# Performance work log

Measured on AMD Instinct MI355X. Metric: run time of the kernel, lower is better.

## Reference

```python
import jax, jax.numpy as jnp
import numpy as np
from jax import lax

B, C_IN, C_OUT, K, H, W, NUM = 32, 256, 256, 3, 28, 28, 8


def setup_inputs() -> dict:
    key = jax.random.key(0)
    k1, k2, k3 = jax.random.split(key, 3)
    inputs = jax.random.normal(k1, (B, C_IN, H, W), dtype=jnp.float32)
    inputs_se = jax.random.uniform(k2, (B, NUM), dtype=jnp.float32)
    # weight bank [out*in*k*k, num], init scale sqrt(1/(c*k*k)) as in the module
    scale = np.sqrt(1.0 / (C_IN * K * K)).astype(np.float32)
    weight = jax.random.normal(k3, (C_OUT * C_IN * K * K, NUM), dtype=jnp.float32) * scale
    bias = jnp.zeros((C_OUT,), dtype=jnp.float32)
    return {"inputs": inputs, "inputs_se": inputs_se, "weight": weight, "bias": bias}


def reference(inputs, inputs_se, weight, bias):
    b, c, h, w = inputs.shape
    out_ch = bias.shape[0]
    # per-sample filter generation: [B, num] @ [num, out*in*k*k] -> [B, out, in, k, k]
    wgen = jnp.einsum('bn,on->bo', inputs_se, weight).reshape(b, out_ch, c, K, K)

    def conv_one(x, wk):
        # x: [C,H,W], wk: [O,C,K,K] -> [O,H,W]  (stride 1, padding 1)
        return lax.conv_general_dilated(
            x[None], wk,
            window_strides=(1, 1), padding=[(1, 1), (1, 1)],
            dimension_numbers=('NCHW', 'OIHW', 'NCHW'))[0]

    out = jax.vmap(conv_one)(inputs, wgen)  # [B, O, H, W]
    return out + bias[None, :, None, None]
```

## Files before the change

kernel.cpp:

```cpp
#include <hip/hip_runtime.h>
#include <hip/hip_fp16.h>

#define BB    32
#define CIN   256
#define COUT  256
#define HH    28
#define WW    28
#define NPIX  784
#define HP    30
#define WP    30

#define BM    128
#define BN    128
#define NT    7

#define SLICE_ELEMS 294912
#define WGEN_ELEMS  ((size_t)BB * 2 * SLICE_ELEMS)
#define XPAD_OFF    (WGEN_ELEMS)

#define PREP_GENW  256
#define PREP_GENX  960
#define PREP_GRID  (PREP_GENW + PREP_GENX)

typedef _Float16 f16x8 __attribute__((ext_vector_type(8)));
typedef float    f32x4 __attribute__((ext_vector_type(4)));

static __device__ __forceinline__ ushort f2h_bits(float v) {
    __half h = __float2half(v);
    return *reinterpret_cast<ushort*>(&h);
}

static __device__ __forceinline__ void gll16(const ushort* g, ushort* l) {
    __builtin_amdgcn_global_load_lds(
        (const __attribute__((address_space(1))) unsigned int*)g,
        (__attribute__((address_space(3))) unsigned int*)l, 16, 0, 0);
}

__global__ __launch_bounds__(256) void prep(const float* __restrict__ weight,
                                            const float* __restrict__ se,
                                            const float* __restrict__ x,
                                            ushort* __restrict__ wgen2,
                                            ushort* __restrict__ xpad) {
    __shared__ __align__(16) char smem[29696];
    const int bid = blockIdx.x;
    const int tid = threadIdx.x;

    if (bid < PREP_GENW) {
        const int og  = bid >> 3;
        const int c32 = bid & 7;
        const int ol  = tid >> 5;
        const int cl  = tid & 31;
        const int o   = og * 8 + ol;
        const int c   = c32 * 32 + cl;
        const int mt  = o >> 7;
        const int sub = (o >> 4) & 7;
        const int col = o & 15;

        float*  se_sh = (float*)smem;
        ushort* w_lds = (ushort*)(smem + 1024);

        se_sh[tid] = se[tid];

        float4 wr[18];
        const float4* wp = (const float4*)(weight + ((size_t)o * CIN + c) * 72);
#pragma unroll
        for (int i = 0; i < 18; ++i) wr[i] = wp[i];

        const int khw0 = tid >> 5;
        const int q0   = (tid >> 3) & 3;
        const int ol0  = tid & 7;
        const int khw1 = 8;
        const int q1   = (tid >> 3) & 3;
        const int ol1  = tid & 7;
        const int o0   = og * 8 + ol0;
        const int sub0 = (o0 >> 4) & 7, col0 = o0 & 15;
        const int o1   = og * 8 + ol1;
        const int sub1 = (o1 >> 4) & 7, col1 = o1 & 15;
        const int dst0 = ((c32 * 9 + khw0) * 512 + sub0 * 64 + q0 * 16 + col0) * 8;
        const int dst1 = ((c32 * 9 + khw1) * 512 + sub1 * 64 + q1 * 16 + col1) * 8;
        const int src0 = (khw0 * 8 + ol0) * 40 + q0 * 8;
        const int src1 = (khw1 * 8 + ol1) * 40 + q1 * 8;

        __syncthreads();

        for (int b = 0; b < BB; ++b) {
            const float s0 = se_sh[b * 8 + 0], s1 = se_sh[b * 8 + 1];
            const float s2 = se_sh[b * 8 + 2], s3 = se_sh[b * 8 + 3];
            const float s4 = se_sh[b * 8 + 4], s5 = se_sh[b * 8 + 5];
            const float s6 = se_sh[b * 8 + 6], s7 = se_sh[b * 8 + 7];
#pragma unroll
            for (int k = 0; k < 9; ++k) {
                const float4 w0 = wr[2 * k + 0];
                const float4 w1 = wr[2 * k + 1];
                const float v = w0.x * s0 + w0.y * s1 + w0.z * s2 + w0.w * s3
                              + w1.x * s4 + w1.y * s5 + w1.z * s6 + w1.w * s7;
                w_lds[(k * 8 + ol) * 40 + cl] = f2h_bits(v);
            }
            __syncthreads();
            ushort* slice_base = wgen2 + (size_t)(b * 2 + mt) * SLICE_ELEMS;
            *(uint4*)(slice_base + dst0) = *(const uint4*)(w_lds + src0);
            if (tid < 32)
                *(uint4*)(slice_base + dst1) = *(const uint4*)(w_lds + src1);
            __syncthreads();
        }
    } else {
        const int idx = bid - PREP_GENW;
        const int hp  = idx % HP;
        const int b   = idx / HP;
        ushort* row = xpad + ((size_t)b * HP + hp) * WP * CIN;

        if (hp == 0 || hp == HP - 1) {
            uint* r32 = (uint*)row;
            for (int i = tid; i < (WP * CIN) / 2; i += 256) r32[i] = 0u;
            return;
        }
        {
            uint* c0 = (uint*)row;
            uint* c1 = (uint*)(row + (WP - 1) * CIN);
            if (tid < 128)       c0[tid] = 0u;
            else                 c1[tid - 128] = 0u;
        }
        float* lds = (float*)smem;
        const int h = hp - 1;
        const float* xr = x + (size_t)b * CIN * NPIX + h * WW;

        for (int f = tid; f < CIN * WW; f += 256) {
            const int c = f / WW;
            const int w = f % WW;
            lds[c * (WW + 1) + w] = xr[(size_t)c * NPIX + w];
        }
        __syncthreads();
        for (int g2 = tid; g2 < WW * CIN; g2 += 256) {
            const int w = g2 >> 8;
            const int c = g2 & 255;
            row[(w + 1) * CIN + c] = f2h_bits(lds[c * (WW + 1) + w]);
        }
    }
}

__global__ __launch_bounds__(256) void dconv_mfma(const ushort* __restrict__ wgen2,
                                                  const ushort* __restrict__ xpad,
                                                  const float* __restrict__ bias,
                                                  float* __restrict__ out) {
    const int bid   = blockIdx.x;
    const int g     = bid & 7;
    const int s     = bid >> 3;
    const int nt    = s % NT;
    const int slice = g + 8 * (s / NT);
    const int b     = slice >> 1;
    const int mt    = slice & 1;

    const int tid  = threadIdx.x;
    const int lane = tid & 63;
    const int wave = tid >> 6;
    const int wm   = wave >> 1;
    const int wn   = wave & 1;
    const int col  = lane & 15;
    const int quad = lane >> 4;

    __shared__ ushort Psh[4 * 8 * 30 * 8];

    const int mo   = mt * BM + wm * 64;
    const int no   = nt * BN + wn * 64;
    const int h_lo = (nt * BN) / WW;

    const f16x8* ag = (const f16x8*)(wgen2 + (size_t)slice * SLICE_ELEMS)
                      + (wm * 4) * 64 + lane;
    const ushort* xp = xpad + (size_t)b * HP * WP * CIN;

    int p_goff[4], p_loff[4];
    bool p_ok[4];
#pragma unroll
    for (int r = 0; r < 4; ++r) {
        const int j = r * 256 + tid;
        p_ok[r] = (j < 960);
        const int jj  = p_ok[r] ? j : 0;
        const int qc  = jj / 240;
        const int rem = jj % 240;
        const int rr  = rem / 30;
        const int ww  = rem % 30;
        int srow = h_lo + rr;
        if (srow > 29) srow = 29;
        p_goff[r] = (srow * WP + ww) * CIN + qc * 8;
        p_loff[r] = jj * 8;
    }

    int pixbase[4], pst[4];
#pragma unroll
    for (int j = 0; j < 4; ++j) {
        const int p  = no + j * 16 + col;
        pst[j] = p;
        const int pc = p > (NPIX - 1) ? (NPIX - 1) : p;
        pixbase[j] = (pc / WW - h_lo) * 30 + (pc % WW);
    }

    f32x4 acc[4][4];
#pragma unroll
    for (int mi = 0; mi < 4; ++mi)
#pragma unroll
        for (int nj = 0; nj < 4; ++nj)
            acc[mi][nj] = (f32x4){0.f, 0.f, 0.f, 0.f};

    for (int c32 = 0; c32 < 8; ++c32) {
        __syncthreads();

#pragma unroll
        for (int r = 0; r < 4; ++r)
            if (p_ok[r]) gll16(xp + p_goff[r] + c32 * 32, Psh + p_loff[r]);
        __syncthreads();

#pragma unroll
        for (int khw = 0; khw < 9; ++khw) {
            const f16x8* a0 = ag + ((c32 * 9 + khw) << 9);
            f16x8 af[4];
#pragma unroll
            for (int mi = 0; mi < 4; ++mi)
                af[mi] = a0[mi * 64];

            const int koff = (khw / 3) * 30 + (khw % 3);
            f16x8 bf[4];
#pragma unroll
            for (int j = 0; j < 4; ++j)
                bf[j] = ((const f16x8*)Psh)[quad * 240 + pixbase[j] + koff];

#pragma unroll
            for (int mi = 0; mi < 4; ++mi)
#pragma unroll
                for (int nj = 0; nj < 4; ++nj)
                    acc[mi][nj] = __builtin_amdgcn_mfma_f32_16x16x32_f16(
                        af[mi], bf[nj], acc[mi][nj], 0, 0, 0);
        }
    }

    float* ob = out + (size_t)b * COUT * NPIX;
#pragma unroll
    for (int mi = 0; mi < 4; ++mi) {
        const int m = mo + mi * 16 + quad * 4;
        const float4 bv = *(const float4*)(bias + m);
#pragma unroll
        for (int nj = 0; nj < 4; ++nj) {
            const int p = pst[nj];
            if (p < NPIX) {
                ob[(size_t)(m + 0) * NPIX + p] = acc[mi][nj][0] + bv.x;
                ob[(size_t)(m + 1) * NPIX + p] = acc[mi][nj][1] + bv.y;
                ob[(size_t)(m + 2) * NPIX + p] = acc[mi][nj][2] + bv.z;
                ob[(size_t)(m + 3) * NPIX + p] = acc[mi][nj][3] + bv.w;
            }
        }
    }
}

extern "C" void kernel_launch(void* const* d_in, const int* in_sizes, int n_in,
                              void* d_out, int out_size, void* d_ws, size_t ws_size,
                              hipStream_t stream) {
    const float* x      = (const float*)d_in[0];
    const float* se     = (const float*)d_in[1];
    const float* weight = (const float*)d_in[2];
    const float* bias   = (const float*)d_in[3];
    float* out          = (float*)d_out;

    ushort* wgen2 = (ushort*)d_ws;
    ushort* xpad  = (ushort*)d_ws + XPAD_OFF;
    (void)ws_size; (void)in_sizes; (void)n_in; (void)out_size;

    prep<<<dim3(PREP_GRID), dim3(256), 0, stream>>>(weight, se, x, wgen2, xpad);
    dconv_mfma<<<dim3(BB * 2 * NT), dim3(256), 0, stream>>>(wgen2, xpad, bias, out);
}
```

Baseline: 151.8 us.

## Double-buffer input tile in LDS and prefetch MFMA operand fragments

The conv kernel now keeps two LDS buffers for the padded input channel slice, so the async global-to-LDS load for the next 32-channel chunk is issued while the current chunk is computed. This removes the second barrier per chunk. Weight (A) fragments are prefetched into a three-deep register ring two steps ahead, and LDS (B) fragments one step ahead, to hide global and LDS latency behind the MFMAs. Launch bounds request two blocks per CU. In exchange the LDS footprint and register pressure go up, which could limit occupancy. The prep kernel change only renames how the output slice index is derived.

```diff
diff --git a/kernel.cpp b/kernel.cpp
--- a/kernel.cpp
+++ b/kernel.cpp
@@ -52,9 +52,6 @@
         const int cl  = tid & 31;
         const int o   = og * 8 + ol;
         const int c   = c32 * 32 + cl;
-        const int mt  = o >> 7;
-        const int sub = (o >> 4) & 7;
-        const int col = o & 15;
 
         float*  se_sh = (float*)smem;
         ushort* w_lds = (ushort*)(smem + 1024);
@@ -76,6 +73,7 @@
         const int sub0 = (o0 >> 4) & 7, col0 = o0 & 15;
         const int o1   = og * 8 + ol1;
         const int sub1 = (o1 >> 4) & 7, col1 = o1 & 15;
+        const int mt0  = o0 >> 7;
         const int dst0 = ((c32 * 9 + khw0) * 512 + sub0 * 64 + q0 * 16 + col0) * 8;
         const int dst1 = ((c32 * 9 + khw1) * 512 + sub1 * 64 + q1 * 16 + col1) * 8;
         const int src0 = (khw0 * 8 + ol0) * 40 + q0 * 8;
@@ -97,7 +95,7 @@
                 w_lds[(k * 8 + ol) * 40 + cl] = f2h_bits(v);
             }
             __syncthreads();
-            ushort* slice_base = wgen2 + (size_t)(b * 2 + mt) * SLICE_ELEMS;
+            ushort* slice_base = wgen2 + (size_t)(b * 2 + mt0) * SLICE_ELEMS;
             *(uint4*)(slice_base + dst0) = *(const uint4*)(w_lds + src0);
             if (tid < 32)
                 *(uint4*)(slice_base + dst1) = *(const uint4*)(w_lds + src1);
@@ -138,10 +136,12 @@
     }
 }
 
-__global__ __launch_bounds__(256) void dconv_mfma(const ushort* __restrict__ wgen2,
-                                                  const ushort* __restrict__ xpad,
-                                                  const float* __restrict__ bias,
-                                                  float* __restrict__ out) {
+#define KOFF(k) (((k) / 3) * 30 + ((k) % 3))
+
+__global__ __launch_bounds__(256, 2) void dconv_mfma(const ushort* __restrict__ wgen2,
+                                                     const ushort* __restrict__ xpad,
+                                                     const float* __restrict__ bias,
+                                                     float* __restrict__ out) {
     const int bid   = blockIdx.x;
     const int g     = bid & 7;
     const int s     = bid >> 3;
@@ -158,7 +158,7 @@
     const int col  = lane & 15;
     const int quad = lane >> 4;
 
-    __shared__ ushort Psh[4 * 8 * 30 * 8];
+    __shared__ ushort Psh[2][7680];
 
     const int mo   = mt * BM + wm * 64;
     const int no   = nt * BN + wn * 64;
@@ -201,34 +201,57 @@
         for (int nj = 0; nj < 4; ++nj)
             acc[mi][nj] = (f32x4){0.f, 0.f, 0.f, 0.f};
 
+#pragma unroll
+    for (int r = 0; r < 4; ++r)
+        if (p_ok[r]) gll16(xp + p_goff[r], &Psh[0][p_loff[r]]);
+
+    f16x8 afr[3][4];
+#pragma unroll
+    for (int mi = 0; mi < 4; ++mi) afr[0][mi] = ag[mi * 64];
+    {
+        const f16x8* a1 = ag + (1 << 9);
+#pragma unroll
+        for (int mi = 0; mi < 4; ++mi) afr[1][mi] = a1[mi * 64];
+    }
+
+    f16x8 bfr[2][4];
+
     for (int c32 = 0; c32 < 8; ++c32) {
         __syncthreads();
 
-#pragma unroll
-        for (int r = 0; r < 4; ++r)
-            if (p_ok[r]) gll16(xp + p_goff[r] + c32 * 32, Psh + p_loff[r]);
-        __syncthreads();
+        if (c32 < 7) {
+            const int nb = (c32 + 1) & 1;
+#pragma unroll
+            for (int r = 0; r < 4; ++r)
+                if (p_ok[r]) gll16(xp + p_goff[r] + (c32 + 1) * 32,
+                                   &Psh[nb][p_loff[r]]);
+        }
+
+        const f16x8* Pc = (const f16x8*)Psh[c32 & 1];
+
+#pragma unroll
+        for (int j = 0; j < 4; ++j)
+            bfr[0][j] = Pc[quad * 240 + pixbase[j] + KOFF(0)];
 
 #pragma unroll
         for (int khw = 0; khw < 9; ++khw) {
-            const f16x8* a0 = ag + ((c32 * 9 + khw) << 9);
-            f16x8 af[4];
+            const int st = c32 * 9 + khw;
+            int sp = st + 2; if (sp > 71) sp = 71;
+            const f16x8* apf = ag + ((size_t)sp << 9);
 #pragma unroll
             for (int mi = 0; mi < 4; ++mi)
-                af[mi] = a0[mi * 64];
-
-            const int koff = (khw / 3) * 30 + (khw % 3);
-            f16x8 bf[4];
-#pragma unroll
-            for (int j = 0; j < 4; ++j)
-                bf[j] = ((const f16x8*)Psh)[quad * 240 + pixbase[j] + koff];
-
+                afr[(khw + 2) % 3][mi] = apf[mi * 64];
+            if (khw < 8) {
+#pragma unroll
+                for (int j = 0; j < 4; ++j)
+                    bfr[(khw + 1) & 1][j] = Pc[quad * 240 + pixbase[j] + KOFF(khw + 1)];
+            }
 #pragma unroll
             for (int mi = 0; mi < 4; ++mi)
 #pragma unroll
                 for (int nj = 0; nj < 4; ++nj)
                     acc[mi][nj] = __builtin_amdgcn_mfma_f32_16x16x32_f16(
-                        af[mi], bf[nj], acc[mi][nj], 0, 0, 0);
+                        afr[khw % 3][mi], bfr[khw & 1][nj], acc[mi][nj], 0, 0, 0);
         }
     }
 
```

Measured after the change: 151.3 us. Within noise of the previous version (-0.3%).
